# Kernel tuning notes

Hardware: AMD Instinct MI355X
Metric: run time of the kernel (lower is better)

The kernel has to match this reference:

```python
import jax, jax.numpy as jnp
from jax import lax
import numpy as np

B = 1024          # batch
N = 30            # max_nodes
IN_DIM = 32       # latent dim
NT, ET = 5, 3     # node / edge type counts
CH = [64, 32, 32, 1]
KS = [(3, 7), (3, 3), (3, 3), (3, 5)]
ST = [(1, 1), (1, 4), (1, 2), (1, 2)]
PD = [(0, 0), (0, 0), (1, 0), (1, 4)]   # torch-style ConvTranspose2d padding
BN_EPS = 1e-5
SMALL = 1e-7


def setup_inputs() -> dict:
    key = jax.random.key(0)
    ks = jax.random.split(key, 5)
    inp = {"Z": jax.random.normal(ks[0], (B, IN_DIM), jnp.float32)}
    cin = [1] + CH[:-1]
    for i in range(4):
        fan_in = KS[i][0] * KS[i][1] * cin[i]
        w = jax.random.normal(ks[i + 1], (KS[i][0], KS[i][1], cin[i], CH[i]), jnp.float32)
        inp[f"W{i+1}"] = w * np.float32(1.0 / np.sqrt(fan_in))
    for i in range(3):
        inp[f"g{i+1}"] = jnp.ones((CH[i],), jnp.float32)
        inp[f"b{i+1}"] = jnp.zeros((CH[i],), jnp.float32)
    return inp


def _deconv(x, w, s, k, p):
    # torch ConvTranspose2d(padding=p) == conv with lhs_dilation=s and pad k-1-p per side
    pads = ((k[0] - 1 - p[0],) * 2, (k[1] - 1 - p[1],) * 2)
    return lax.conv_transpose(x, w, s, pads, dimension_numbers=("NHWC", "HWIO", "NHWC"))


def _bn_relu(x, g, b):
    m = x.mean((0, 1, 2))
    v = x.var((0, 1, 2))
    return jax.nn.relu(g * (x - m) * lax.rsqrt(v + BN_EPS) + b)


def _generator(Z, Ws, gbs):
    x = Z.reshape(B, IN_DIM, 1, 1)                      # NHWC: (B, 32, 1, 1)
    for i in range(4):
        x = _deconv(x, Ws[i], ST[i], KS[i], PD[i])
        if i < 3:
            x = _bn_relu(x, *gbs[i])
    return x.reshape(B, N, -1)                          # (B, 30, 126)


def reference(Z, W1, W2, W3, W4, g1, b1, g2, b2, g3, b3):
    out = _generator(Z, (W1, W2, W3, W4), ((g1, b1), (g2, b2), (g3, b3)))
    X = jax.nn.softmax(out[:, :, : NT + 1], axis=-1)    # (B, N, 6) soft node types
    iu = jnp.triu_indices(N, 1)                         # 435 upper-triangular edges
    oe = out[:, :, NT + 1:].reshape(B, N, N, ET + 1)[:, iu[0], iu[1], :]
    ve = jax.nn.softmax(oe, axis=-1)                    # (B, 435, 4) soft edge types
    all_edges = jnp.stack(iu).astype(jnp.int32)         # (2, 435)
    edge_index = jnp.concatenate([all_edges, all_edges[::-1]], axis=-1)  # (2, 870)
    batch = jnp.repeat(jnp.arange(B), N)
    edge_attr = jnp.concatenate([ve, ve], axis=1)       # (B, 870, 4)
    # vectorized hard selection: one fused argmax->one-hot pass instead of O(B*N) python loops
    X_hard = jax.nn.one_hot(jnp.argmax(X, axis=-1), NT + 1, dtype=X.dtype)
    ve_hard = jax.nn.one_hot(jnp.argmax(ve, axis=-1), ET + 1, dtype=ve.dtype)
    ea_hard = jnp.concatenate([ve_hard, ve_hard], axis=1)
    log_prob = (jnp.sum(jnp.log(X + SMALL) * X_hard)
                + jnp.sum(jnp.log(ve + SMALL) * ve_hard))
    return (X[:, :, 1:], edge_index, edge_attr[:, :, 1:],
            1.0 - X[:, :, 0], 1.0 - edge_attr[:, :, 0], batch,
            X_hard[:, :, 1:], ea_hard[:, :, 1:],
            1.0 - X_hard[:, :, 0], 1.0 - ea_hard[:, :, 0], log_prob)
```

## Files before the change

kernel.cpp:

```cpp
#include <hip/hip_runtime.h>
#include <hip/hip_bf16.h>

typedef __hip_bfloat16 bf16;
typedef __attribute__((ext_vector_type(8))) short short8;
typedef __attribute__((ext_vector_type(4))) float floatx4;
typedef __bf16 bf16x8 __attribute__((ext_vector_type(8)));

#define OFF_A1 0
#define OFF_C1 64
#define OFF_A2 128
#define OFF_C2 160
#define OFF_A3 192
#define OFF_C3 224
#define OFF_LP 256
#define OFF_P1S 512
#define OFF_P1Q 66048
#define OFF_P2S 131584
#define OFF_P2Q 205312
#define OFF_P3S 279040
#define OFF_P3Q 426496
#define FLT_END 573952

#define FW2_BYTE 2295808u
#define FW3_BYTE 2332672u
#define FW4_BYTE 2351104u
#define X2_BYTE  33546240u
#define X3_BYTE  97247232u
#define O4_BYTE  227008512u

#define OUT0 0
#define OUT1 153600
#define OUT2 155340
#define OUT3 2827980
#define OUT4 2858700
#define OUT5 3749580
#define OUT6 3780300
#define OUT7 3933900
#define OUT8 6606540
#define OUT9 6637260
#define OUT10 7528140

__device__ __forceinline__ bf16 f2b(float v){ return __float2bfloat16(v); }
__device__ __forceinline__ unsigned short f2bu(float v){ bf16 h = __float2bfloat16(v); return *(unsigned short*)&h; }

__device__ __forceinline__ floatx4 mfma16(short8 a, short8 b, floatx4 c){
  return __builtin_amdgcn_mfma_f32_16x16x32_bf16(__builtin_bit_cast(bf16x8, a),
                                                 __builtin_bit_cast(bf16x8, b), c, 0, 0, 0);
}

__device__ __forceinline__ unsigned int nrm2(unsigned int u, float a0, float c0, float a1, float c1){
  float x0 = __uint_as_float(u << 16);
  float x1 = __uint_as_float(u & 0xffff0000u);
  float y0 = fmaxf(fmaf(a0, x0, c0), 0.f);
  float y1 = fmaxf(fmaf(a1, x1, c1), 0.f);
  return (unsigned int)f2bu(y0) | ((unsigned int)f2bu(y1) << 16);
}

__global__ __launch_bounds__(256) void k_prep(const float* __restrict__ W2, const float* __restrict__ W3,
                                              const float* __restrict__ W4,
                                              unsigned short* __restrict__ fw2, unsigned short* __restrict__ fw3,
                                              unsigned short* __restrict__ fw4){
  const int t = blockIdx.x*256 + threadIdx.x;
  if (t < 2304){
    const int L = t & 63, kc = (t>>6)&1, mt = (t>>7)&1, tap = t>>8;
    const int co = mt*16 + (L&15), ci0 = kc*32 + ((L>>4)&3)*8;
    #pragma unroll
    for (int j = 0; j < 8; ++j)
      fw2[(size_t)t*8 + j] = f2bu(W2[((size_t)tap*64 + ci0 + j)*32 + co]);
  }
  if (t < 1152){
    const int L = t & 63, mt = (t>>6)&1, tap = t>>7;
    const int co = mt*16 + (L&15), ci0 = ((L>>4)&3)*8;
    #pragma unroll
    for (int j = 0; j < 8; ++j)
      fw3[(size_t)t*8 + j] = f2bu(W3[((size_t)tap*32 + ci0 + j)*32 + co]);
  }
  if (t < 1920){
    const int L = t & 63, d = (t>>6) % 10, r = t / 640;
    const int m = L & 15, ci0 = ((L>>4)&3)*8;
    const int kw = 2*d - m;
    #pragma unroll
    for (int j = 0; j < 8; ++j)
      fw4[(size_t)t*8 + j] = (kw >= 0 && kw < 5) ? f2bu(W4[(r*5 + kw)*32 + ci0 + j])
                                                 : (unsigned short)0;
  }
}

__global__ __launch_bounds__(256) void k_dc1(const float* __restrict__ Z, const float* __restrict__ W1,
                                             float* __restrict__ ws){
  const int b = blockIdx.x, t = threadIdx.x;
  __shared__ float zs[32];
  __shared__ float w1s[3*7*64];
  __shared__ float red[256];
  if (t < 32) zs[t] = Z[b*32 + t];
  for (int i = t; i < 1344; i += 256) w1s[i] = W1[i];
  __syncthreads();
  float lsum = 0.f, lsq = 0.f;
  for (int idx = t; idx < 15232; idx += 256){
    int co = idx & 63;
    int wo = (idx >> 6) % 7;
    int ho = idx / 448;
    int kw = 6 - wo;
    float y = 0.f;
    #pragma unroll
    for (int kh = 0; kh < 3; ++kh){
      int hi = ho + kh - 2;
      if (hi >= 0 && hi < 32) y += zs[hi] * w1s[(kh*7 + kw)*64 + co];
    }
    lsum += y; lsq += y*y;
  }
  red[t] = lsum; __syncthreads();
  if (t < 64) ws[OFF_P1S + b*64 + t] = red[t] + red[t+64] + red[t+128] + red[t+192];
  __syncthreads();
  red[t] = lsq; __syncthreads();
  if (t < 64) ws[OFF_P1Q + b*64 + t] = red[t] + red[t+64] + red[t+128] + red[t+192];
}

__global__ __launch_bounds__(256) void k_fin(float* __restrict__ ws, const float* __restrict__ g,
                                             const float* __restrict__ bb, int ps, int pq, int npart,
                                             int nch, float inv_n, int ao, int co, int zlp){
  const int c = blockIdx.x, t = threadIdx.x;
  __shared__ float r1[256], r2[256];
  float s = 0.f, q = 0.f;
  for (int i = t; i < npart; i += 256){ s += ws[ps + i*nch + c]; q += ws[pq + i*nch + c]; }
  r1[t] = s; r2[t] = q; __syncthreads();
  for (int off = 128; off > 0; off >>= 1){
    if (t < off){ r1[t] += r1[t+off]; r2[t] += r2[t+off]; }
    __syncthreads();
  }
  if (t == 0){
    float m  = r1[0] * inv_n;
    float v  = r2[0] * inv_n - m*m;
    float is = rsqrtf(v + 1e-5f);
    float a  = g[c] * is;
    ws[ao + c] = a;
    ws[co + c] = bb[c] - a*m;
  }
  if (zlp && c == 0 && t == 0) ws[OFF_LP] = 0.f;
}

__global__ __launch_bounds__(256) void k2(const float* __restrict__ Z, const float* __restrict__ W1,
                                          const unsigned short* __restrict__ fw2,
                                          unsigned short* __restrict__ x2, float* __restrict__ ws){
  const int t = threadIdx.x;
  const int b0 = blockIdx.x*16, ho = blockIdx.y;
  __shared__ unsigned short sa[21*1024];
  __shared__ float zs[16][32];
  __shared__ float w1s[1344];
  __shared__ float sa1[64], sc1[64];
  __shared__ float sred[2][4][32];
  if (t < 64){ sa1[t] = ws[OFF_A1+t]; sc1[t] = ws[OFF_C1+t]; }
  for (int i = t; i < 512; i += 256) zs[i>>5][i&31] = Z[(b0 + (i>>5))*32 + (i&31)];
  for (int i = t; i < 1344; i += 256) w1s[i] = W1[i];
  __syncthreads();
  for (int c = t; c < 21*128; c += 256){
    const int p = c >> 7, g = c & 127;
    const int r = p/7, wi = p - r*7;
    const int hi = ho - 2 + r;
    const int b = g >> 3, kc = (g >> 2) & 1, j = g & 3;
    const int ci0 = kc*32 + j*8;
    unsigned int pk[4] = {0,0,0,0};
    if (hi >= 0 && hi < 34){
      const float* wp = &w1s[(6 - wi)*64 + ci0];
      #pragma unroll
      for (int e = 0; e < 8; e += 2){
        float y0 = 0.f, y1 = 0.f;
        #pragma unroll
        for (int kh = 0; kh < 3; ++kh){
          const int q = hi + kh - 2;
          if (q >= 0 && q < 32){
            float zv = zs[b][q];
            y0 += zv * wp[kh*448 + e];
            y1 += zv * wp[kh*448 + e + 1];
          }
        }
        float u0 = fmaxf(fmaf(sa1[ci0+e],   y0, sc1[ci0+e]),   0.f);
        float u1 = fmaxf(fmaf(sa1[ci0+e+1], y1, sc1[ci0+e+1]), 0.f);
        pk[e>>1] = (unsigned int)f2bu(u0) | ((unsigned int)f2bu(u1) << 16);
      }
    }
    *(uint4*)(sa + (size_t)p*1024 + kc*512 + (j*16 + b)*8) = *(uint4*)pk;
  }
  __syncthreads();
  const int w = t>>6, L = t&63;
  floatx4 acc[8][2];
  #pragma unroll
  for (int i = 0; i < 8; ++i){ acc[i][0] = (floatx4)0.f; acc[i][1] = (floatx4)0.f; }
  const int wiA = 2*w, wiB = (w < 3) ? 2*w + 1 : 2*w;
  for (int r = 0; r < 3; ++r){
    short8 af[3][2][2];
    #pragma unroll
    for (int kw = 0; kw < 3; ++kw)
      #pragma unroll
      for (int mt = 0; mt < 2; ++mt)
        #pragma unroll
        for (int kc = 0; kc < 2; ++kc)
          af[kw][mt][kc] = *(const short8*)(fw2 + ((((size_t)(r*3+kw)*2 + mt)*2 + kc)*64 + L)*8);
    const short8* pA = (const short8*)(sa + (size_t)(r*7 + wiA)*1024);
    const short8* pB = (const short8*)(sa + (size_t)(r*7 + wiB)*1024);
    short8 fa0 = pA[L], fa1 = pA[64+L];
    short8 fb0 = pB[L], fb1 = pB[64+L];
    #pragma unroll
    for (int idx = 0; idx < 8; ++idx){
      if (idx == 3 || idx == 7) continue;
      const int kw = (2 - idx) & 3;
      const int half = idx >> 2;
      if (half && w == 3) continue;
      short8 f0 = half ? fb0 : fa0;
      short8 f1 = half ? fb1 : fa1;
      #pragma unroll
      for (int mt = 0; mt < 2; ++mt){
        acc[idx][mt] = mfma16(af[kw][mt][0], f0, acc[idx][mt]);
        acc[idx][mt] = mfma16(af[kw][mt][1], f1, acc[idx][mt]);
      }
    }
  }
  const int bL = L & 15, jj = (L>>4)&3;
  float ss[2][4] = {{0,0,0,0},{0,0,0,0}}, sq[2][4] = {{0,0,0,0},{0,0,0,0}};
  #pragma unroll
  for (int idx = 0; idx < 8; ++idx){
    if (8*w + idx >= 27) continue;
    #pragma unroll
    for (int mt = 0; mt < 2; ++mt){
      floatx4 a = acc[idx][mt];
      ss[mt][0] += a.x; ss[mt][1] += a.y; ss[mt][2] += a.z; ss[mt][3] += a.w;
      sq[mt][0] += a.x*a.x; sq[mt][1] += a.y*a.y; sq[mt][2] += a.z*a.z; sq[mt][3] += a.w*a.w;
    }
  }
  #pragma unroll
  for (int mt = 0; mt < 2; ++mt)
    #pragma unroll
    for (int r2 = 0; r2 < 4; ++r2){
      float v1 = ss[mt][r2], v2 = sq[mt][r2];
      for (int d = 1; d < 16; d <<= 1){ v1 += __shfl_xor(v1, d, 64); v2 += __shfl_xor(v2, d, 64); }
      if (bL == 0){
        int cch = mt*16 + jj*4 + r2;
        sred[0][w][cch] = v1;
        sred[1][w][cch] = v2;
      }
    }
  __syncthreads();
  if (t < 64){
    const int cch = t & 31, j2 = t >> 5;
    float tot = sred[j2][0][cch] + sred[j2][1][cch] + sred[j2][2][cch] + sred[j2][3][cch];
    const int bid = blockIdx.y*64 + blockIdx.x;
    ws[(j2 ? OFF_P2Q : OFF_P2S) + bid*32 + cch] = tot;
  }
  unsigned short* st = sa + w*4608;
  #pragma unroll
  for (int idx = 0; idx < 8; ++idx){
    if (8*w + idx >= 27) continue;
    #pragma unroll
    for (int mt = 0; mt < 2; ++mt){
      floatx4 a = acc[idx][mt];
      uint2 pk;
      pk.x = (unsigned int)f2bu(a.x) | ((unsigned int)f2bu(a.y) << 16);
      pk.y = (unsigned int)f2bu(a.z) | ((unsigned int)f2bu(a.w) << 16);
      *(uint2*)(st + idx*576 + bL*36 + mt*16 + jj*4) = pk;
    }
  }
  const int sb = L >> 2, q2 = L & 3;
  #pragma unroll
  for (int idx = 0; idx < 8; ++idx){
    const int wo = 8*w + idx;
    if (wo >= 27) continue;
    uint4 v = *(const uint4*)(st + idx*576 + sb*36 + q2*8);
    *(uint4*)(x2 + ((size_t)(ho*27+wo)*1024 + b0 + sb)*32 + q2*8) = v;
  }
}

__global__ __launch_bounds__(256) void k3(const unsigned short* __restrict__ x2, const unsigned short* __restrict__ fw3,
                                          unsigned short* __restrict__ x3, float* __restrict__ ws){
  const int t = threadIdx.x;
  const int b0 = blockIdx.x*16, ho = blockIdx.y, z = blockIdx.z;
  const int wib = z*15;
  __shared__ unsigned short sa[48*512];
  __shared__ float sa2[32], sc2[32];
  __shared__ float sred[2][4][32];
  if (t < 32){ sa2[t] = ws[OFF_A2+t]; sc2[t] = ws[OFF_C2+t]; }
  __syncthreads();
  for (int c = t; c < 48*64; c += 256){
    const int p = c >> 6, g = c & 63;
    const int r = p >> 4, wl = p & 15;
    const int wi = wib + wl;
    const int hi = ho - 1 + r;
    const int b = g >> 2, j = g & 3;
    const int ci0 = j*8;
    uint4 v = make_uint4(0,0,0,0);
    if (hi >= 0 && hi < 36 && wi < 27){
      v = *(const uint4*)(x2 + ((size_t)(hi*27+wi)*1024 + b0 + b)*32 + ci0);
      v.x = nrm2(v.x, sa2[ci0],   sc2[ci0],   sa2[ci0+1], sc2[ci0+1]);
      v.y = nrm2(v.y, sa2[ci0+2], sc2[ci0+2], sa2[ci0+3], sc2[ci0+3]);
      v.z = nrm2(v.z, sa2[ci0+4], sc2[ci0+4], sa2[ci0+5], sc2[ci0+5]);
      v.w = nrm2(v.w, sa2[ci0+6], sc2[ci0+6], sa2[ci0+7], sc2[ci0+7]);
    }
    *(uint4*)(sa + (size_t)p*512 + (j*16 + b)*8) = v;
  }
  __syncthreads();
  const int w = t>>6, L = t&63;
  const int s0 = z ? (32 + 6*w) : (8*w);
  const int h2 = s0 >> 1;
  const int nvalid = z ? ((w == 3) ? 5 : 6) : 8;
  floatx4 acc[8][2];
  #pragma unroll
  for (int i = 0; i < 8; ++i){ acc[i][0] = (floatx4)0.f; acc[i][1] = (floatx4)0.f; }
  for (int r = 0; r < 3; ++r){
    short8 af[3][2];
    #pragma unroll
    for (int kw = 0; kw < 3; ++kw)
      #pragma unroll
      for (int mt = 0; mt < 2; ++mt)
        af[kw][mt] = *(const short8*)(fw3 + (((size_t)(r*3+kw)*2 + mt)*64 + L)*8);
    short8 bb[5];
    #pragma unroll
    for (int d = 0; d < 5; ++d){
      const int wi = h2 - 1 + d;
      short8 v = (short8)0;
      if (wi >= 0 && wi < 27)
        v = *(const short8*)(sa + (size_t)(r*16 + wi - wib)*512 + L*8);
      bb[d] = v;
    }
    #pragma unroll
    for (int idx = 0; idx < 8; ++idx){
      if (idx >= nvalid) continue;
      if ((idx & 1) == 0){
        const int d = idx >> 1;
        #pragma unroll
        for (int mt = 0; mt < 2; ++mt){
          acc[idx][mt] = mfma16(af[0][mt], bb[d],   acc[idx][mt]);
          acc[idx][mt] = mfma16(af[2][mt], bb[d+1], acc[idx][mt]);
        }
      } else {
        const int d = ((idx - 1) >> 1) + 1;
        #pragma unroll
        for (int mt = 0; mt < 2; ++mt)
          acc[idx][mt] = mfma16(af[1][mt], bb[d], acc[idx][mt]);
      }
    }
  }
  const int bL = L & 15, jj = (L>>4)&3;
  float ss[2][4] = {{0,0,0,0},{0,0,0,0}}, sq[2][4] = {{0,0,0,0},{0,0,0,0}};
  #pragma unroll
  for (int idx = 0; idx < 8; ++idx){
    if (idx >= nvalid) continue;
    #pragma unroll
    for (int mt = 0; mt < 2; ++mt){
      floatx4 a = acc[idx][mt];
      ss[mt][0] += a.x; ss[mt][1] += a.y; ss[mt][2] += a.z; ss[mt][3] += a.w;
      sq[mt][0] += a.x*a.x; sq[mt][1] += a.y*a.y; sq[mt][2] += a.z*a.z; sq[mt][3] += a.w*a.w;
    }
  }
  #pragma unroll
  for (int mt = 0; mt < 2; ++mt)
    #pragma unroll
    for (int r2 = 0; r2 < 4; ++r2){
      float v1 = ss[mt][r2], v2 = sq[mt][r2];
      for (int d = 1; d < 16; d <<= 1){ v1 += __shfl_xor(v1, d, 64); v2 += __shfl_xor(v2, d, 64); }
      if (bL == 0){
        int cch = mt*16 + jj*4 + r2;
        sred[0][w][cch] = v1;
        sred[1][w][cch] = v2;
      }
    }
  __syncthreads();
  if (t < 64){
    const int cch = t & 31, j2 = t >> 5;
    float tot = sred[j2][0][cch] + sred[j2][1][cch] + sred[j2][2][cch] + sred[j2][3][cch];
    const int bid = (z*36 + blockIdx.y)*64 + blockIdx.x;
    ws[(j2 ? OFF_P3Q : OFF_P3S) + bid*32 + cch] = tot;
  }
  unsigned short* st = sa + w*4608;
  #pragma unroll
  for (int idx = 0; idx < 8; ++idx){
    if (idx >= nvalid) continue;
    #pragma unroll
    for (int mt = 0; mt < 2; ++mt){
      floatx4 a = acc[idx][mt];
      uint2 pk;
      pk.x = (unsigned int)f2bu(a.x) | ((unsigned int)f2bu(a.y) << 16);
      pk.y = (unsigned int)f2bu(a.z) | ((unsigned int)f2bu(a.w) << 16);
      *(uint2*)(st + idx*576 + bL*36 + mt*16 + jj*4) = pk;
    }
  }
  const int sb = L >> 2, q2 = L & 3;
  #pragma unroll
  for (int idx = 0; idx < 8; ++idx){
    if (idx >= nvalid) continue;
    const int wo = s0 + idx;
    uint4 v = *(const uint4*)(st + idx*576 + sb*36 + q2*8);
    *(uint4*)(x3 + ((size_t)(ho*55+wo)*1024 + b0 + sb)*32 + q2*8) = v;
  }
}

__global__ __launch_bounds__(256) void k_dc4(const unsigned short* __restrict__ x3,
                                             const unsigned short* __restrict__ fw4,
                                             float* __restrict__ o4, const float* __restrict__ ws){
  const int t = threadIdx.x;
  const int w = t >> 6, L = t & 63;
  const int b0 = blockIdx.x*16;
  const int ho0 = blockIdx.y*3;
  __shared__ float a3s[32], c3s[32];
  __shared__ unsigned short fa4[30*512];
  __shared__ float rowbuf[16*113];
  if (t < 32){ a3s[t] = ws[OFF_A3+t]; c3s[t] = ws[OFF_C3+t]; }
  for (int i = t; i < 1920; i += 256)
    *(uint4*)(fa4 + (size_t)i*8) = *(const uint4*)(fw4 + (size_t)i*8);
  __syncthreads();
  const int bL = L & 15, jj = (L>>4)&3, ci0 = jj*8;
  float an[8], cn[8];
  #pragma unroll
  for (int e = 0; e < 8; ++e){ an[e] = a3s[ci0+e]; cn[e] = c3s[ci0+e]; }
  floatx4 acc[2][3];
  #pragma unroll
  for (int i = 0; i < 2; ++i)
    #pragma unroll
    for (int h = 0; h < 3; ++h) acc[i][h] = (floatx4)0.f;
  #pragma unroll
  for (int ts = 0; ts < 2; ++ts){
    const int T = w + ts*4;
    if (T >= 7) continue;
    const int dmax = (T == 6) ? 7 : 10;
    #pragma unroll
    for (int e = 0; e < 5; ++e){
      const int hi = ho0 - 1 + e;
      if (hi < 0 || hi >= 36) continue;
      for (int d = 0; d < dmax; ++d){
        const int wi = 8*T + d;
        uint4 v = *(const uint4*)(x3 + ((size_t)(hi*55 + wi)*1024 + b0 + bL)*32 + ci0);
        v.x = nrm2(v.x, an[0], cn[0], an[1], cn[1]);
        v.y = nrm2(v.y, an[2], cn[2], an[3], cn[3]);
        v.z = nrm2(v.z, an[4], cn[4], an[5], cn[5]);
        v.w = nrm2(v.w, an[6], cn[6], an[7], cn[7]);
        short8 bf = __builtin_bit_cast(short8, v);
        #pragma unroll
        for (int hl = 0; hl < 3; ++hl){
          const int r = e - hl;
          if (r < 0 || r > 2) continue;
          short8 af = *(const short8*)(fa4 + ((size_t)(r*10 + d)*64 + L)*8);
          acc[ts][hl] = mfma16(af, bf, acc[ts][hl]);
        }
      }
    }
  }
  #pragma unroll
  for (int hl = 0; hl < 3; ++hl){
    __syncthreads();
    #pragma unroll
    for (int ts = 0; ts < 2; ++ts){
      const int T = w + ts*4;
      if (T >= 7) continue;
      floatx4 a = acc[ts][hl];
      float vals[4] = {a.x, a.y, a.z, a.w};
      #pragma unroll
      for (int reg = 0; reg < 4; ++reg){
        const int wo = 16*T + jj*4 + reg;
        if (wo < 105) rowbuf[bL*113 + wo] = vals[reg];
      }
    }
    __syncthreads();
    const int ho = ho0 + hl;
    for (int i = t; i < 1680; i += 256){
      const int bb = i / 105, wo = i - bb*105;
      o4[(size_t)(b0 + bb)*3780 + ho*105 + wo] = rowbuf[bb*113 + wo];
    }
  }
}

__global__ __launch_bounds__(256) void k_node(const float* __restrict__ o4, float* __restrict__ dout,
                                              float* __restrict__ ws){
  const int t = threadIdx.x;
  const int tg = blockIdx.x*256 + t;
  __shared__ float red[256];
  float lp = 0.f;
  {
    int b = tg / 30, n = tg - b*30;
    const float* p = o4 + (size_t)b*3780 + n*126;
    float l[6]; float mx = -1e30f;
    #pragma unroll
    for (int j = 0; j < 6; ++j){ l[j] = p[j]; mx = fmaxf(mx, l[j]); }
    float e[6]; float s = 0.f;
    #pragma unroll
    for (int j = 0; j < 6; ++j){ e[j] = expf(l[j] - mx); s += e[j]; }
    float inv = 1.f / s;
    int am = 0; float best = e[0];
    #pragma unroll
    for (int j = 1; j < 6; ++j){ if (e[j] > best){ best = e[j]; am = j; } }
    #pragma unroll
    for (int j = 0; j < 5; ++j) dout[OUT0 + (size_t)tg*5 + j] = e[j+1]*inv;
    dout[OUT3 + tg] = 1.f - e[0]*inv;
    #pragma unroll
    for (int j = 0; j < 5; ++j) dout[OUT6 + (size_t)tg*5 + j] = (am == j+1) ? 1.f : 0.f;
    dout[OUT8 + tg] = (am != 0) ? 1.f : 0.f;
    dout[OUT5 + tg] = (float)b;
    lp = logf(best*inv + 1e-7f);
  }
  red[t] = lp; __syncthreads();
  for (int off = 128; off > 0; off >>= 1){ if (t < off) red[t] += red[t+off]; __syncthreads(); }
  if (t == 0) atomicAdd(&ws[OFF_LP], red[0]);
}

__global__ __launch_bounds__(256) void k_edge(const float* __restrict__ o4, float* __restrict__ dout,
                                              float* __restrict__ ws){
  const int t = threadIdx.x;
  const int tg = blockIdx.x*256 + t;
  __shared__ float red[256];
  float lp = 0.f;
  {
    int b = tg / 435, k = tg - b*435;
    int i = 0, rem = k;
    while (rem >= 29 - i){ rem -= 29 - i; ++i; }
    int j = i + 1 + rem;
    const float* p = o4 + (size_t)b*3780 + i*126 + 6 + j*4;
    float l0 = p[0], l1 = p[1], l2 = p[2], l3 = p[3];
    float mx = fmaxf(fmaxf(l0, l1), fmaxf(l2, l3));
    float e0 = expf(l0-mx), e1 = expf(l1-mx), e2 = expf(l2-mx), e3 = expf(l3-mx);
    float inv = 1.f / (e0 + e1 + e2 + e3);
    float pr0 = e0*inv, pr1 = e1*inv, pr2 = e2*inv, pr3 = e3*inv;
    int am = 0; float best = pr0;
    if (pr1 > best){ best = pr1; am = 1; }
    if (pr2 > best){ best = pr2; am = 2; }
    if (pr3 > best){ best = pr3; am = 3; }
    size_t e1i = (size_t)b*870 + k, e2i = e1i + 435;
    dout[OUT2 + e1i*3 + 0] = pr1; dout[OUT2 + e1i*3 + 1] = pr2; dout[OUT2 + e1i*3 + 2] = pr3;
    dout[OUT2 + e2i*3 + 0] = pr1; dout[OUT2 + e2i*3 + 1] = pr2; dout[OUT2 + e2i*3 + 2] = pr3;
    dout[OUT4 + e1i] = 1.f - pr0;  dout[OUT4 + e2i] = 1.f - pr0;
    float h1 = (am == 1) ? 1.f : 0.f, h2 = (am == 2) ? 1.f : 0.f, h3 = (am == 3) ? 1.f : 0.f;
    dout[OUT7 + e1i*3 + 0] = h1; dout[OUT7 + e1i*3 + 1] = h2; dout[OUT7 + e1i*3 + 2] = h3;
    dout[OUT7 + e2i*3 + 0] = h1; dout[OUT7 + e2i*3 + 1] = h2; dout[OUT7 + e2i*3 + 2] = h3;
    dout[OUT9 + e1i] = (am != 0) ? 1.f : 0.f;  dout[OUT9 + e2i] = (am != 0) ? 1.f : 0.f;
    if (b == 0){
      dout[OUT1 + k]        = (float)i;
      dout[OUT1 + 435 + k]  = (float)j;
      dout[OUT1 + 870 + k]  = (float)j;
      dout[OUT1 + 1305 + k] = (float)i;
    }
    lp = logf(best + 1e-7f);
  }
  red[t] = lp; __syncthreads();
  for (int off = 128; off > 0; off >>= 1){ if (t < off) red[t] += red[t+off]; __syncthreads(); }
  if (t == 0) atomicAdd(&ws[OFF_LP], red[0]);
}

__global__ void k_lp_copy(float* __restrict__ dout, const float* __restrict__ ws){
  if (threadIdx.x == 0 && blockIdx.x == 0) dout[OUT10] = ws[OFF_LP];
}

extern "C" void kernel_launch(void* const* d_in, const int* in_sizes, int n_in,
                              void* d_out, int out_size, void* d_ws, size_t ws_size,
                              hipStream_t stream) {
  const float* Z  = (const float*)d_in[0];
  const float* W1 = (const float*)d_in[1];
  const float* W2 = (const float*)d_in[2];
  const float* W3 = (const float*)d_in[3];
  const float* W4 = (const float*)d_in[4];
  const float* g1 = (const float*)d_in[5];
  const float* b1 = (const float*)d_in[6];
  const float* g2 = (const float*)d_in[7];
  const float* b2 = (const float*)d_in[8];
  const float* g3 = (const float*)d_in[9];
  const float* b3 = (const float*)d_in[10];

  float* ws  = (float*)d_ws;
  char*  wsb = (char*)d_ws;
  unsigned short* fw2 = (unsigned short*)(wsb + FW2_BYTE);
  unsigned short* fw3 = (unsigned short*)(wsb + FW3_BYTE);
  unsigned short* fw4 = (unsigned short*)(wsb + FW4_BYTE);
  unsigned short* x2u = (unsigned short*)(wsb + X2_BYTE);
  unsigned short* x3u = (unsigned short*)(wsb + X3_BYTE);
  float*          o4  = (float*)(wsb + O4_BYTE);
  float* dout = (float*)d_out;
  (void)in_sizes; (void)n_in; (void)out_size; (void)ws_size;

  k_prep<<<dim3(9), dim3(256), 0, stream>>>(W2, W3, W4, fw2, fw3, fw4);
  k_dc1<<<dim3(1024), dim3(256), 0, stream>>>(Z, W1, ws);
  k_fin<<<dim3(64), dim3(256), 0, stream>>>(ws, g1, b1, OFF_P1S, OFF_P1Q, 1024, 64,
                                            1.f/243712.f, OFF_A1, OFF_C1, 0);
  k2<<<dim3(64, 36), dim3(256), 0, stream>>>(Z, W1, fw2, x2u, ws);
  k_fin<<<dim3(32), dim3(256), 0, stream>>>(ws, g2, b2, OFF_P2S, OFF_P2Q, 2304, 32,
                                            1.f/995328.f, OFF_A2, OFF_C2, 0);
  k3<<<dim3(64, 36, 2), dim3(256), 0, stream>>>(x2u, fw3, x3u, ws);
  k_fin<<<dim3(32), dim3(256), 0, stream>>>(ws, g3, b3, OFF_P3S, OFF_P3Q, 4608, 32,
                                            1.f/2027520.f, OFF_A3, OFF_C3, 1);
  k_dc4<<<dim3(64, 12), dim3(256), 0, stream>>>(x3u, fw4, o4, ws);
  k_node<<<dim3(120), dim3(256), 0, stream>>>(o4, dout, ws);
  k_edge<<<dim3(1740), dim3(256), 0, stream>>>(o4, dout, ws);
  k_lp_copy<<<dim3(1), dim3(64), 0, stream>>>(dout, ws);
}
```

Baseline: 339.8 us.

## Split layer-3 deconv into three column tiles with async global-to-LDS staging

The layer-3 transposed-conv kernel now splits the width into three tiles instead of two, shrinking its LDS footprint and per-wave accumulator count to raise occupancy. Input staging uses global_load_lds direct copies followed by an in-place LDS normalize pass. The partial-stats buffers move to a new workspace offset to fit the extra blocks. The layer-4 kernel reorders its loops to be row-outer with a fixed trip count and a bounds guard, and the edge kernel replaces its triangular-index while loop with a closed-form sqrt. The extra LDS pass and a larger halo overlap fraction add some redundant work.

```diff
diff --git a/kernel.cpp b/kernel.cpp
--- a/kernel.cpp
+++ b/kernel.cpp
@@ -17,9 +17,6 @@
 #define OFF_P1Q 66048
 #define OFF_P2S 131584
 #define OFF_P2Q 205312
-#define OFF_P3S 279040
-#define OFF_P3Q 426496
-#define FLT_END 573952
 
 #define FW2_BYTE 2295808u
 #define FW3_BYTE 2332672u
@@ -27,6 +24,9 @@
 #define X2_BYTE  33546240u
 #define X3_BYTE  97247232u
 #define O4_BYTE  227008512u
+
+#define P3S_ABS 56752128
+#define P3Q_ABS 56973312
 
 #define OUT0 0
 #define OUT1 153600
@@ -54,6 +54,11 @@
   float y0 = fmaxf(fmaf(a0, x0, c0), 0.f);
   float y1 = fmaxf(fmaf(a1, x1, c1), 0.f);
   return (unsigned int)f2bu(y0) | ((unsigned int)f2bu(y1) << 16);
+}
+
+__device__ __forceinline__ void gload_lds16(const unsigned short* g, unsigned short* lds){
+  __builtin_amdgcn_global_load_lds((const __attribute__((address_space(1))) unsigned int*)g,
+                                   (__attribute__((address_space(3))) unsigned int*)lds, 16, 0, 0);
 }
 
 __global__ __launch_bounds__(256) void k_prep(const float* __restrict__ W2, const float* __restrict__ W3,
@@ -273,37 +278,50 @@
                                           unsigned short* __restrict__ x3, float* __restrict__ ws){
   const int t = threadIdx.x;
   const int b0 = blockIdx.x*16, ho = blockIdx.y, z = blockIdx.z;
-  const int wib = z*15;
-  __shared__ unsigned short sa[48*512];
+  const int wib = (z == 0) ? 0 : ((z == 1) ? 8 : 17);
+  __shared__ unsigned short sa[33*512];
   __shared__ float sa2[32], sc2[32];
   __shared__ float sred[2][4][32];
   if (t < 32){ sa2[t] = ws[OFF_A2+t]; sc2[t] = ws[OFF_C2+t]; }
-  __syncthreads();
-  for (int c = t; c < 48*64; c += 256){
-    const int p = c >> 6, g = c & 63;
-    const int r = p >> 4, wl = p & 15;
-    const int wi = wib + wl;
-    const int hi = ho - 1 + r;
-    const int b = g >> 2, j = g & 3;
-    const int ci0 = j*8;
-    uint4 v = make_uint4(0,0,0,0);
+  const int w = t>>6, L = t&63;
+  const int bL = L & 15, jL = (L>>4)&3, ci0 = jL*8;
+  for (int p = w; p < 33; p += 4){
+    const int r = p/11, wl = p - r*11;
+    const int hi = ho - 1 + r, wi = wib + wl;
+    unsigned short* dst = sa + p*512;
     if (hi >= 0 && hi < 36 && wi < 27){
-      v = *(const uint4*)(x2 + ((size_t)(hi*27+wi)*1024 + b0 + b)*32 + ci0);
-      v.x = nrm2(v.x, sa2[ci0],   sc2[ci0],   sa2[ci0+1], sc2[ci0+1]);
-      v.y = nrm2(v.y, sa2[ci0+2], sc2[ci0+2], sa2[ci0+3], sc2[ci0+3]);
-      v.z = nrm2(v.z, sa2[ci0+4], sc2[ci0+4], sa2[ci0+5], sc2[ci0+5]);
-      v.w = nrm2(v.w, sa2[ci0+6], sc2[ci0+6], sa2[ci0+7], sc2[ci0+7]);
-    }
-    *(uint4*)(sa + (size_t)p*512 + (j*16 + b)*8) = v;
-  }
-  __syncthreads();
-  const int w = t>>6, L = t&63;
-  const int s0 = z ? (32 + 6*w) : (8*w);
+      const unsigned short* src = x2 + ((size_t)(hi*27 + wi)*1024 + b0 + bL)*32 + ci0;
+      gload_lds16(src, dst);
+    } else {
+      *(uint4*)(dst + L*8) = make_uint4(0,0,0,0);
+    }
+  }
+  __syncthreads();
+  {
+    float an[8], cn[8];
+    #pragma unroll
+    for (int e = 0; e < 8; ++e){ an[e] = sa2[ci0+e]; cn[e] = sc2[ci0+e]; }
+    for (int i = t; i < 2112; i += 256){
+      const int p = i >> 6;
+      const int r = p/11, wl = p - r*11;
+      const int hi = ho - 1 + r, wi = wib + wl;
+      if (hi >= 0 && hi < 36 && wi < 27){
+        uint4 v = *(uint4*)(sa + (size_t)i*8);
+        v.x = nrm2(v.x, an[0], cn[0], an[1], cn[1]);
+        v.y = nrm2(v.y, an[2], cn[2], an[3], cn[3]);
+        v.z = nrm2(v.z, an[4], cn[4], an[5], cn[5]);
+        v.w = nrm2(v.w, an[6], cn[6], an[7], cn[7]);
+        *(uint4*)(sa + (size_t)i*8) = v;
+      }
+    }
+  }
+  __syncthreads();
+  const int s0 = z*18 + ((w==0) ? 0 : (w==1) ? 6 : (w==2) ? 10 : 14);
   const int h2 = s0 >> 1;
-  const int nvalid = z ? ((w == 3) ? 5 : 6) : 8;
-  floatx4 acc[8][2];
-  #pragma unroll
-  for (int i = 0; i < 8; ++i){ acc[i][0] = (floatx4)0.f; acc[i][1] = (floatx4)0.f; }
+  const int nvalid = (w==0) ? 6 : ((z==2 && w==3) ? 5 : 4);
+  floatx4 acc[6][2];
+  #pragma unroll
+  for (int i = 0; i < 6; ++i){ acc[i][0] = (floatx4)0.f; acc[i][1] = (floatx4)0.f; }
   for (int r = 0; r < 3; ++r){
     short8 af[3][2];
     #pragma unroll
@@ -311,17 +329,18 @@
       #pragma unroll
       for (int mt = 0; mt < 2; ++mt)
         af[kw][mt] = *(const short8*)(fw3 + (((size_t)(r*3+kw)*2 + mt)*64 + L)*8);
-    short8 bb[5];
-    #pragma unroll
-    for (int d = 0; d < 5; ++d){
+    short8 bb[4];
+    #pragma unroll
+    for (int d = 0; d < 4; ++d){
       const int wi = h2 - 1 + d;
+      const int wl = wi - wib;
       short8 v = (short8)0;
-      if (wi >= 0 && wi < 27)
-        v = *(const short8*)(sa + (size_t)(r*16 + wi - wib)*512 + L*8);
+      if (wl >= 0 && wl <= 10)
+        v = *(const short8*)(sa + (size_t)(r*11 + wl)*512 + L*8);
       bb[d] = v;
     }
     #pragma unroll
-    for (int idx = 0; idx < 8; ++idx){
+    for (int idx = 0; idx < 6; ++idx){
       if (idx >= nvalid) continue;
       if ((idx & 1) == 0){
         const int d = idx >> 1;
@@ -338,10 +357,10 @@
       }
     }
   }
-  const int bL = L & 15, jj = (L>>4)&3;
+  const int jj = jL;
   float ss[2][4] = {{0,0,0,0},{0,0,0,0}}, sq[2][4] = {{0,0,0,0},{0,0,0,0}};
   #pragma unroll
-  for (int idx = 0; idx < 8; ++idx){
+  for (int idx = 0; idx < 6; ++idx){
     if (idx >= nvalid) continue;
     #pragma unroll
     for (int mt = 0; mt < 2; ++mt){
@@ -367,11 +386,11 @@
     const int cch = t & 31, j2 = t >> 5;
     float tot = sred[j2][0][cch] + sred[j2][1][cch] + sred[j2][2][cch] + sred[j2][3][cch];
     const int bid = (z*36 + blockIdx.y)*64 + blockIdx.x;
-    ws[(j2 ? OFF_P3Q : OFF_P3S) + bid*32 + cch] = tot;
-  }
-  unsigned short* st = sa + w*4608;
-  #pragma unroll
-  for (int idx = 0; idx < 8; ++idx){
+    ws[(j2 ? P3Q_ABS : P3S_ABS) + bid*32 + cch] = tot;
+  }
+  unsigned short* st = sa + w*3456;
+  #pragma unroll
+  for (int idx = 0; idx < 6; ++idx){
     if (idx >= nvalid) continue;
     #pragma unroll
     for (int mt = 0; mt < 2; ++mt){
@@ -384,7 +403,7 @@
   }
   const int sb = L >> 2, q2 = L & 3;
   #pragma unroll
-  for (int idx = 0; idx < 8; ++idx){
+  for (int idx = 0; idx < 6; ++idx){
     if (idx >= nvalid) continue;
     const int wo = s0 + idx;
     uint4 v = *(const uint4*)(st + idx*576 + sb*36 + q2*8);
@@ -415,23 +434,27 @@
   for (int i = 0; i < 2; ++i)
     #pragma unroll
     for (int h = 0; h < 3; ++h) acc[i][h] = (floatx4)0.f;
-  #pragma unroll
-  for (int ts = 0; ts < 2; ++ts){
-    const int T = w + ts*4;
-    if (T >= 7) continue;
-    const int dmax = (T == 6) ? 7 : 10;
-    #pragma unroll
-    for (int e = 0; e < 5; ++e){
-      const int hi = ho0 - 1 + e;
-      if (hi < 0 || hi >= 36) continue;
-      for (int d = 0; d < dmax; ++d){
+  for (int e = 0; e < 5; ++e){
+    const int hi = ho0 - 1 + e;
+    if (hi < 0 || hi >= 36) continue;
+    #pragma unroll
+    for (int ts = 0; ts < 2; ++ts){
+      const int T = w + ts*4;
+      if (T >= 7) continue;
+      #pragma unroll 5
+      for (int d = 0; d < 10; ++d){
         const int wi = 8*T + d;
-        uint4 v = *(const uint4*)(x3 + ((size_t)(hi*55 + wi)*1024 + b0 + bL)*32 + ci0);
-        v.x = nrm2(v.x, an[0], cn[0], an[1], cn[1]);
-        v.y = nrm2(v.y, an[2], cn[2], an[3], cn[3]);
-        v.z = nrm2(v.z, an[4], cn[4], an[5], cn[5]);
-        v.w = nrm2(v.w, an[6], cn[6], an[7], cn[7]);
-        short8 bf = __builtin_bit_cast(short8, v);
+        short8 bf;
+        if (wi < 55){
+          uint4 v = *(const uint4*)(x3 + ((size_t)(hi*55 + wi)*1024 + b0 + bL)*32 + ci0);
+          v.x = nrm2(v.x, an[0], cn[0], an[1], cn[1]);
+          v.y = nrm2(v.y, an[2], cn[2], an[3], cn[3]);
+          v.z = nrm2(v.z, an[4], cn[4], an[5], cn[5]);
+          v.w = nrm2(v.w, an[6], cn[6], an[7], cn[7]);
+          bf = __builtin_bit_cast(short8, v);
+        } else {
+          bf = (short8)0;
+        }
         #pragma unroll
         for (int hl = 0; hl < 3; ++hl){
           const int r = e - hl;
@@ -507,8 +530,10 @@
   float lp = 0.f;
   {
     int b = tg / 435, k = tg - b*435;
-    int i = 0, rem = k;
-    while (rem >= 29 - i){ rem -= 29 - i; ++i; }
+    int i = (int)((59.0f - sqrtf((float)(3481 - 8*k))) * 0.5f);
+    int rem = k - ((i*(59 - i)) >> 1);
+    if (rem < 0){ i -= 1; rem = k - ((i*(59 - i)) >> 1); }
+    else if (rem >= 29 - i){ rem -= 29 - i; i += 1; }
     int j = i + 1 + rem;
     const float* p = o4 + (size_t)b*3780 + i*126 + 6 + j*4;
     float l0 = p[0], l1 = p[1], l2 = p[2], l3 = p[3];
@@ -578,8 +603,8 @@
   k2<<<dim3(64, 36), dim3(256), 0, stream>>>(Z, W1, fw2, x2u, ws);
   k_fin<<<dim3(32), dim3(256), 0, stream>>>(ws, g2, b2, OFF_P2S, OFF_P2Q, 2304, 32,
                                             1.f/995328.f, OFF_A2, OFF_C2, 0);
-  k3<<<dim3(64, 36, 2), dim3(256), 0, stream>>>(x2u, fw3, x3u, ws);
-  k_fin<<<dim3(32), dim3(256), 0, stream>>>(ws, g3, b3, OFF_P3S, OFF_P3Q, 4608, 32,
+  k3<<<dim3(64, 36, 3), dim3(256), 0, stream>>>(x2u, fw3, x3u, ws);
+  k_fin<<<dim3(32), dim3(256), 0, stream>>>(ws, g3, b3, P3S_ABS, P3Q_ABS, 6912, 32,
                                             1.f/2027520.f, OFF_A3, OFF_C3, 1);
   k_dc4<<<dim3(64, 12), dim3(256), 0, stream>>>(x3u, fw4, o4, ws);
   k_node<<<dim3(120), dim3(256), 0, stream>>>(o4, dout, ws);
```

Result: slower. 361.5 us (+6.4%).
